# Optimization experiments

Hardware: AMD Instinct MI355X
Metric: run time of the kernel (lower is better)

Reference implementation:

```python
import jax, jax.numpy as jnp
import numpy as np

LAYER_NUM = 4
INPUT_DIM = 1024
BATCH = 16384


def setup_inputs() -> dict:
    key = jax.random.key(0)
    k1, k2, k3 = jax.random.split(key, 3)
    x = jax.random.normal(k1, (BATCH, INPUT_DIM), dtype=jnp.float32)
    cross_weights = jax.random.normal(k2, (LAYER_NUM, INPUT_DIM), dtype=jnp.float32)
    cross_bias = jax.random.normal(k3, (LAYER_NUM, INPUT_DIM), dtype=jnp.float32)
    return {"x": x, "cross_weights": cross_weights, "cross_bias": cross_bias}


def reference(x, cross_weights, cross_bias):
    # Faithful DCN cross network:
    #   x_{i+1} = x0 @ x_i^T @ w_i + b_i + x_i
    # The [B,d,d] outer product bmm collapses to a per-row scalar dot:
    #   x_{i+1} = x0 * (x_i . w_i) + b_i + x_i
    x0 = x
    xi = x
    for i in range(LAYER_NUM):
        s = xi @ cross_weights[i]            # [B]  (x_i^T w_i)
        xi = x0 * s[:, None] + cross_bias[i] + xi  # [B, d]
    return xi
```

## Files before the change

### kernel.cpp

```cpp
#include <hip/hip_runtime.h>


#define D 1024
#define CHUNKS 4
#define ITER 4

typedef float nfloat4 __attribute__((ext_vector_type(4)));

__global__ __launch_bounds__(256) void cross_pipe_kernel(
    const float* __restrict__ x,
    const float* __restrict__ w,
    const float* __restrict__ b,
    float* __restrict__ out,
    int batch)
{
    const int wid  = (int)((blockIdx.x * blockDim.x + threadIdx.x) >> 6);
    const int lane = (int)(threadIdx.x & 63);
    const int row0 = wid * ITER;
    if (row0 >= batch) return;

    const float4* w4 = (const float4*)w;
    const float4* b4 = (const float4*)b;

    float g1 = 0.f, g2 = 0.f, g3 = 0.f;
    float4 Bsum[CHUNKS];
#pragma unroll
    for (int c = 0; c < CHUNKS; ++c) {
        const int idx = c * 64 + lane;
        float4 bb0 = b4[idx], bb1 = b4[256 + idx];
        float4 bb2 = b4[512 + idx], bb3 = b4[768 + idx];
        float4 wv1 = w4[256 + idx], wv2 = w4[512 + idx], wv3 = w4[768 + idx];

        float4 B2, B3, Bs;
        B2.x = bb0.x + bb1.x; B2.y = bb0.y + bb1.y;
        B2.z = bb0.z + bb1.z; B2.w = bb0.w + bb1.w;
        B3.x = B2.x + bb2.x;  B3.y = B2.y + bb2.y;
        B3.z = B2.z + bb2.z;  B3.w = B2.w + bb2.w;
        Bs.x = B3.x + bb3.x;  Bs.y = B3.y + bb3.y;
        Bs.z = B3.z + bb3.z;  Bs.w = B3.w + bb3.w;
        Bsum[c] = Bs;

        g1 = fmaf(bb0.x, wv1.x, g1); g1 = fmaf(bb0.y, wv1.y, g1);
        g1 = fmaf(bb0.z, wv1.z, g1); g1 = fmaf(bb0.w, wv1.w, g1);
        g2 = fmaf(B2.x,  wv2.x, g2); g2 = fmaf(B2.y,  wv2.y, g2);
        g2 = fmaf(B2.z,  wv2.z, g2); g2 = fmaf(B2.w,  wv2.w, g2);
        g3 = fmaf(B3.x,  wv3.x, g3); g3 = fmaf(B3.y,  wv3.y, g3);
        g3 = fmaf(B3.z,  wv3.z, g3); g3 = fmaf(B3.w,  wv3.w, g3);
    }
#pragma unroll
    for (int off = 32; off > 0; off >>= 1) {
        g1 += __shfl_xor(g1, off, 64);
        g2 += __shfl_xor(g2, off, 64);
        g3 += __shfl_xor(g3, off, 64);
    }

    float4 xc[CHUNKS], xn[CHUNKS];
    {
        const float4* row = (const float4*)(x + (size_t)row0 * D);
#pragma unroll
        for (int c = 0; c < CHUNKS; ++c) xc[c] = row[c * 64 + lane];
    }

#pragma unroll 1
    for (int i = 0; i < ITER; ++i) {
        const int rowi = row0 + i;
        const int nrow = (rowi + 1 < batch) ? (rowi + 1) : rowi;
        const float4* nrp = (const float4*)(x + (size_t)nrow * D);
#pragma unroll
        for (int c = 0; c < CHUNKS; ++c) xn[c] = nrp[c * 64 + lane];

        float d0 = 0.f, d1 = 0.f, d2 = 0.f, d3 = 0.f;
#pragma unroll
        for (int c = 0; c < CHUNKS; ++c) {
            const int idx = c * 64 + lane;
            float4 wv0 = w4[idx];
            float4 wv1 = w4[256 + idx];
            float4 wv2 = w4[512 + idx];
            float4 wv3 = w4[768 + idx];
            d0 = fmaf(xc[c].x, wv0.x, d0); d1 = fmaf(xc[c].x, wv1.x, d1);
            d2 = fmaf(xc[c].x, wv2.x, d2); d3 = fmaf(xc[c].x, wv3.x, d3);
            d0 = fmaf(xc[c].y, wv0.y, d0); d1 = fmaf(xc[c].y, wv1.y, d1);
            d2 = fmaf(xc[c].y, wv2.y, d2); d3 = fmaf(xc[c].y, wv3.y, d3);
            d0 = fmaf(xc[c].z, wv0.z, d0); d1 = fmaf(xc[c].z, wv1.z, d1);
            d2 = fmaf(xc[c].z, wv2.z, d2); d3 = fmaf(xc[c].z, wv3.z, d3);
            d0 = fmaf(xc[c].w, wv0.w, d0); d1 = fmaf(xc[c].w, wv1.w, d1);
            d2 = fmaf(xc[c].w, wv2.w, d2); d3 = fmaf(xc[c].w, wv3.w, d3);
        }

#pragma unroll
        for (int off = 32; off > 0; off >>= 1) {
            d0 += __shfl_xor(d0, off, 64);
            d1 += __shfl_xor(d1, off, 64);
            d2 += __shfl_xor(d2, off, 64);
            d3 += __shfl_xor(d3, off, 64);
        }

        float c1 = 1.f + d0;
        float c2 = c1 + fmaf(c1, d1, g1);
        float c3 = c2 + fmaf(c2, d2, g2);
        float c4 = c3 + fmaf(c3, d3, g3);

        nfloat4* orow = (nfloat4*)(out + (size_t)rowi * D);
#pragma unroll
        for (int c = 0; c < CHUNKS; ++c) {
            const int idx = c * 64 + lane;
            nfloat4 o;
            o.x = fmaf(c4, xc[c].x, Bsum[c].x);
            o.y = fmaf(c4, xc[c].y, Bsum[c].y);
            o.z = fmaf(c4, xc[c].z, Bsum[c].z);
            o.w = fmaf(c4, xc[c].w, Bsum[c].w);
            __builtin_nontemporal_store(o, &orow[idx]);
        }

#pragma unroll
        for (int c = 0; c < CHUNKS; ++c) xc[c] = xn[c];
    }
}

extern "C" void kernel_launch(void* const* d_in, const int* in_sizes, int n_in,
                              void* d_out, int out_size, void* d_ws, size_t ws_size,
                              hipStream_t stream) {
    const float* x = (const float*)d_in[0];
    const float* w = (const float*)d_in[1];
    const float* b = (const float*)d_in[2];
    float* out = (float*)d_out;

    const int batch = in_sizes[0] / D;
    const int rows_per_block = ITER * (256 / 64);
    const int grid = (batch + rows_per_block - 1) / rows_per_block;
    cross_pipe_kernel<<<grid, 256, 0, stream>>>(x, w, b, out, batch);
}
```

Measured before the change: 120.1 us.

## Process four rows per wave in parallel with sixteen lanes per row

```diff
diff --git a/kernel.cpp b/kernel.cpp
--- a/kernel.cpp
+++ b/kernel.cpp
@@ -2,30 +2,41 @@
 
 
 #define D 1024
-#define CHUNKS 4
-#define ITER 4
+#define NV4 (D / 4)
+#define RPW 4
+#define LPR 16
+#define CPL (NV4 / LPR)
 
 typedef float nfloat4 __attribute__((ext_vector_type(4)));
 
-__global__ __launch_bounds__(256) void cross_pipe_kernel(
+__global__ __launch_bounds__(256, 4) void cross_flat_kernel(
     const float* __restrict__ x,
     const float* __restrict__ w,
     const float* __restrict__ b,
     float* __restrict__ out,
     int batch)
 {
-    const int wid  = (int)((blockIdx.x * blockDim.x + threadIdx.x) >> 6);
-    const int lane = (int)(threadIdx.x & 63);
-    const int row0 = wid * ITER;
+    __shared__ float4 ldsB[4][NV4];
+
+    const int tid  = (int)threadIdx.x;
+    const int wvid = tid >> 6;
+    const int lane = tid & 63;
+    const int wid  = (int)blockIdx.x * 4 + wvid;
+    const int row0 = wid * RPW;
     if (row0 >= batch) return;
+
+    const int r = lane >> 4;
+    const int t = lane & 15;
+    int rr = row0 + r;
+    if (rr >= batch) rr = batch - 1;
+    const int row = rr;
 
     const float4* w4 = (const float4*)w;
     const float4* b4 = (const float4*)b;
 
     float g1 = 0.f, g2 = 0.f, g3 = 0.f;
-    float4 Bsum[CHUNKS];
 #pragma unroll
-    for (int c = 0; c < CHUNKS; ++c) {
+    for (int c = 0; c < 4; ++c) {
         const int idx = c * 64 + lane;
         float4 bb0 = b4[idx], bb1 = b4[256 + idx];
         float4 bb2 = b4[512 + idx], bb3 = b4[768 + idx];
@@ -38,7 +49,7 @@
         B3.z = B2.z + bb2.z;  B3.w = B2.w + bb2.w;
         Bs.x = B3.x + bb3.x;  Bs.y = B3.y + bb3.y;
         Bs.z = B3.z + bb3.z;  Bs.w = B3.w + bb3.w;
-        Bsum[c] = Bs;
+        ldsB[wvid][idx] = Bs;
 
         g1 = fmaf(bb0.x, wv1.x, g1); g1 = fmaf(bb0.y, wv1.y, g1);
         g1 = fmaf(bb0.z, wv1.z, g1); g1 = fmaf(bb0.w, wv1.w, g1);
@@ -47,6 +58,12 @@
         g3 = fmaf(B3.x,  wv3.x, g3); g3 = fmaf(B3.y,  wv3.y, g3);
         g3 = fmaf(B3.z,  wv3.z, g3); g3 = fmaf(B3.w,  wv3.w, g3);
     }
+
+    const float4* xr = (const float4*)x + (size_t)row * NV4;
+    float4 xv[CPL];
+#pragma unroll
+    for (int c = 0; c < CPL; ++c) xv[c] = xr[c * LPR + t];
+
 #pragma unroll
     for (int off = 32; off > 0; off >>= 1) {
         g1 += __shfl_xor(g1, off, 64);
@@ -54,66 +71,49 @@
         g3 += __shfl_xor(g3, off, 64);
     }
 
-    float4 xc[CHUNKS], xn[CHUNKS];
-    {
-        const float4* row = (const float4*)(x + (size_t)row0 * D);
+    float d0 = 0.f, d1 = 0.f, d2 = 0.f, d3 = 0.f;
 #pragma unroll
-        for (int c = 0; c < CHUNKS; ++c) xc[c] = row[c * 64 + lane];
+    for (int c = 0; c < CPL; ++c) {
+        const int wi = c * LPR + t;
+        float4 wv0 = w4[wi];
+        float4 wv1 = w4[256 + wi];
+        float4 wv2 = w4[512 + wi];
+        float4 wv3 = w4[768 + wi];
+        float4 xc = xv[c];
+        d0 = fmaf(xc.x, wv0.x, d0); d1 = fmaf(xc.x, wv1.x, d1);
+        d2 = fmaf(xc.x, wv2.x, d2); d3 = fmaf(xc.x, wv3.x, d3);
+        d0 = fmaf(xc.y, wv0.y, d0); d1 = fmaf(xc.y, wv1.y, d1);
+        d2 = fmaf(xc.y, wv2.y, d2); d3 = fmaf(xc.y, wv3.y, d3);
+        d0 = fmaf(xc.z, wv0.z, d0); d1 = fmaf(xc.z, wv1.z, d1);
+        d2 = fmaf(xc.z, wv2.z, d2); d3 = fmaf(xc.z, wv3.z, d3);
+        d0 = fmaf(xc.w, wv0.w, d0); d1 = fmaf(xc.w, wv1.w, d1);
+        d2 = fmaf(xc.w, wv2.w, d2); d3 = fmaf(xc.w, wv3.w, d3);
     }
 
-#pragma unroll 1
-    for (int i = 0; i < ITER; ++i) {
-        const int rowi = row0 + i;
-        const int nrow = (rowi + 1 < batch) ? (rowi + 1) : rowi;
-        const float4* nrp = (const float4*)(x + (size_t)nrow * D);
 #pragma unroll
-        for (int c = 0; c < CHUNKS; ++c) xn[c] = nrp[c * 64 + lane];
+    for (int off = 8; off > 0; off >>= 1) {
+        d0 += __shfl_xor(d0, off, 64);
+        d1 += __shfl_xor(d1, off, 64);
+        d2 += __shfl_xor(d2, off, 64);
+        d3 += __shfl_xor(d3, off, 64);
+    }
 
-        float d0 = 0.f, d1 = 0.f, d2 = 0.f, d3 = 0.f;
+    const float c1 = 1.f + d0;
+    const float c2 = c1 + fmaf(c1, d1, g1);
+    const float c3 = c2 + fmaf(c2, d2, g2);
+    const float c4 = c3 + fmaf(c3, d3, g3);
+
+    nfloat4* orow = (nfloat4*)out + (size_t)row * NV4;
 #pragma unroll
-        for (int c = 0; c < CHUNKS; ++c) {
-            const int idx = c * 64 + lane;
-            float4 wv0 = w4[idx];
-            float4 wv1 = w4[256 + idx];
-            float4 wv2 = w4[512 + idx];
-            float4 wv3 = w4[768 + idx];
-            d0 = fmaf(xc[c].x, wv0.x, d0); d1 = fmaf(xc[c].x, wv1.x, d1);
-            d2 = fmaf(xc[c].x, wv2.x, d2); d3 = fmaf(xc[c].x, wv3.x, d3);
-            d0 = fmaf(xc[c].y, wv0.y, d0); d1 = fmaf(xc[c].y, wv1.y, d1);
-            d2 = fmaf(xc[c].y, wv2.y, d2); d3 = fmaf(xc[c].y, wv3.y, d3);
-            d0 = fmaf(xc[c].z, wv0.z, d0); d1 = fmaf(xc[c].z, wv1.z, d1);
-            d2 = fmaf(xc[c].z, wv2.z, d2); d3 = fmaf(xc[c].z, wv3.z, d3);
-            d0 = fmaf(xc[c].w, wv0.w, d0); d1 = fmaf(xc[c].w, wv1.w, d1);
-            d2 = fmaf(xc[c].w, wv2.w, d2); d3 = fmaf(xc[c].w, wv3.w, d3);
-        }
-
-#pragma unroll
-        for (int off = 32; off > 0; off >>= 1) {
-            d0 += __shfl_xor(d0, off, 64);
-            d1 += __shfl_xor(d1, off, 64);
-            d2 += __shfl_xor(d2, off, 64);
-            d3 += __shfl_xor(d3, off, 64);
-        }
-
-        float c1 = 1.f + d0;
-        float c2 = c1 + fmaf(c1, d1, g1);
-        float c3 = c2 + fmaf(c2, d2, g2);
-        float c4 = c3 + fmaf(c3, d3, g3);
-
-        nfloat4* orow = (nfloat4*)(out + (size_t)rowi * D);
-#pragma unroll
-        for (int c = 0; c < CHUNKS; ++c) {
-            const int idx = c * 64 + lane;
-            nfloat4 o;
-            o.x = fmaf(c4, xc[c].x, Bsum[c].x);
-            o.y = fmaf(c4, xc[c].y, Bsum[c].y);
-            o.z = fmaf(c4, xc[c].z, Bsum[c].z);
-            o.w = fmaf(c4, xc[c].w, Bsum[c].w);
-            __builtin_nontemporal_store(o, &orow[idx]);
-        }
-
-#pragma unroll
-        for (int c = 0; c < CHUNKS; ++c) xc[c] = xn[c];
+    for (int c = 0; c < CPL; ++c) {
+        const int wi = c * LPR + t;
+        float4 Bs = ldsB[wvid][wi];
+        nfloat4 o;
+        o.x = fmaf(c4, xv[c].x, Bs.x);
+        o.y = fmaf(c4, xv[c].y, Bs.y);
+        o.z = fmaf(c4, xv[c].z, Bs.z);
+        o.w = fmaf(c4, xv[c].w, Bs.w);
+        __builtin_nontemporal_store(o, &orow[wi]);
     }
 }
 
@@ -126,7 +126,7 @@
     float* out = (float*)d_out;
 
     const int batch = in_sizes[0] / D;
-    const int rows_per_block = ITER * (256 / 64);
+    const int rows_per_block = RPW * (256 / 64);
     const int grid = (batch + rows_per_block - 1) / rows_per_block;
-    cross_pipe_kernel<<<grid, 256, 0, stream>>>(x, w, b, out, batch);
+    cross_flat_kernel<<<grid, 256, 0, stream>>>(x, w, b, out, batch);
 }
```

Result: no change. 122.4 us (+1.9%).
